# Optimization experiments

Hardware: AMD Instinct MI355X
Metric: run time of the kernel (lower is better)

Reference implementation:

```python
import jax, jax.numpy as jnp
import numpy as np

B, S, D, H = 2, 2048, 1024, 16
HD = D // H


def setup_inputs() -> dict:
    key = jax.random.key(0)
    ks = jax.random.split(key, 6)
    std = 1.0 / np.sqrt(D)
    return {
        "hidden_states": jax.random.normal(ks[0], (B, S, D), dtype=jnp.float32),
        "attention_mask": jnp.zeros((B, 1, S, S), dtype=jnp.float32),
        "Wq": jax.random.normal(ks[1], (D, D), dtype=jnp.float32) * std,
        "bq": jnp.zeros((D,), dtype=jnp.float32),
        "Wk": jax.random.normal(ks[2], (D, D), dtype=jnp.float32) * std,
        "bk": jnp.zeros((D,), dtype=jnp.float32),
        "Wv": jax.random.normal(ks[3], (D, D), dtype=jnp.float32) * std,
        "bv": jnp.zeros((D,), dtype=jnp.float32),
        "Wo": jax.random.normal(ks[4], (D, D), dtype=jnp.float32) * std,
        "bo": jnp.zeros((D,), dtype=jnp.float32),
    }


def reference(hidden_states, attention_mask, Wq, bq, Wk, bk, Wv, bv, Wo, bo):
    scale = HD ** (-0.5)
    # torch Linear: y = x @ W^T + b
    def proj(x, W, b):
        y = jnp.einsum('bsd,ed->bse', x, W) + b
        return y.reshape(B, S, H, HD).transpose(0, 2, 1, 3)  # [B,H,S,HD]
    q = proj(hidden_states, Wq, bq)
    k = proj(hidden_states, Wk, bk)
    v = proj(hidden_states, Wv, bv)
    scores = jnp.einsum('bhqd,bhkd->bhqk', q, k) * scale + attention_mask
    attn = jax.nn.softmax(scores, axis=-1)  # dropout p=0.0 -> identity
    out = jnp.einsum('bhqk,bhkd->bhqd', attn, v)
    out = out.transpose(0, 2, 1, 3).reshape(B, S, D)
    return jnp.einsum('bsd,ed->bse', out, Wo) + bo
```

## Files before the change

### kernel.cpp

```cpp
#include <hip/hip_runtime.h>
#include <hip/hip_bf16.h>
#include <stdint.h>

#define Bb 2
#define Ss 2048
#define Dd 1024
#define Hh 16
#define HD 64

typedef __attribute__((ext_vector_type(8))) __bf16 bf16x8;
typedef __attribute__((ext_vector_type(4))) __bf16 bf16x4;
typedef __attribute__((ext_vector_type(2))) __bf16 bf16x2;
typedef __attribute__((ext_vector_type(4))) float f32x4;
typedef __attribute__((ext_vector_type(16))) float f32x16;

#define LOG2E 1.44269504088896f
#define SCL2 (0.125f * LOG2E)

#define HS_N   (Bb * Ss * Dd)
#define W_N    (Dd * Dd)
#define B_N    (Dd)
#define MS_N   ((long)Bb * Ss * Ss)
#define CAN_HS 0
#define CAN_WQ (CAN_HS + HS_N)
#define CAN_BQ (CAN_WQ + W_N)
#define CAN_WK (CAN_BQ + B_N)
#define CAN_BK (CAN_WK + W_N)
#define CAN_WV (CAN_BK + B_N)
#define CAN_BV (CAN_WV + W_N)
#define CAN_WO (CAN_BV + B_N)
#define CAN_BO (CAN_WO + W_N)
#define CAN_END (CAN_BO + B_N)
#define TSZ    (Bb * Hh * Ss * HD)
#define WS_ELEMS (CAN_END + 4 * TSZ)
#define WS_NEED ((size_t)WS_ELEMS * 2)

__device__ __forceinline__ void gl_lds16(const __bf16* g, __bf16* l) {
  __builtin_amdgcn_global_load_lds(
      (const __attribute__((address_space(1))) void*)g,
      (__attribute__((address_space(3))) void*)l,
      16, 0, 0);
}

__device__ __forceinline__ void cfence() { asm volatile("" ::: "memory"); }

__global__ void canon_kernel(const float* hs, const float* Wq, const float* bq,
                             const float* Wk, const float* bk, const float* Wv,
                             const float* bv, const float* Wo, const float* bo,
                             __bf16* __restrict__ dst) {
  const float* srcs[9] = {hs, Wq, bq, Wk, bk, Wv, bv, Wo, bo};
  const long starts[10] = {CAN_HS, CAN_WQ, CAN_BQ, CAN_WK, CAN_BK,
                           CAN_WV, CAN_BV, CAN_WO, CAN_BO, CAN_END};
  const long nA = CAN_END / 8;
  for (long c = blockIdx.x * blockDim.x + threadIdx.x; c < nA;
       c += (long)gridDim.x * blockDim.x) {
    const long i = c * 8;
    int seg = 0;
#pragma unroll
    for (int t = 1; t < 9; t++) seg += (i >= starts[t]) ? 1 : 0;
    const float* s = srcs[seg] + (i - starts[seg]);
    bf16x8 v;
#pragma unroll
    for (int e = 0; e < 8; e++) v[e] = (__bf16)s[e];
    *(bf16x8*)(dst + i) = v;
  }
}

template <int MODE, typename OutT>
__global__ __launch_bounds__(256, 2) void gemm_bt(
    const __bf16* __restrict__ A,
    const __bf16* __restrict__ W0, const __bf16* __restrict__ W1,
    const __bf16* __restrict__ W2,
    const __bf16* __restrict__ b0, const __bf16* __restrict__ b1,
    const __bf16* __restrict__ b2,
    OutT* __restrict__ O0, OutT* __restrict__ O1, OutT* __restrict__ O2,
    const float* __restrict__ Mf, __bf16* __restrict__ Mout) {
  constexpr int TN = (MODE == 1) ? 64 : 128;
  constexpr int NACC = TN / 32;
  __shared__ __align__(16) __bf16 sA[2][128 * 32];
  __shared__ __align__(16) __bf16 sB[2][TN * 32];
  const int tid = threadIdx.x;

  if (MODE == 0 && blockIdx.y >= 24) {
    const long nT = (long)Bb * 32 * 32 * 256;
    const long t0 = ((long)(blockIdx.y - 24) * 32 + blockIdx.x) * 256 + tid;
    for (long tc = t0; tc < nT; tc += 65536) {
      const int t = (int)(tc & 255);
      const long tile = tc >> 8;
      const int kvt = (int)(tile & 31);
      const int qt = (int)((tile >> 5) & 31);
      const int b = (int)(tile >> 10);
      const int l31 = t & 31, hi5 = (t >> 5) & 1;
      const int qg = (t >> 6) & 1, kvh = (t >> 7) & 1;
      const int q = qt * 64 + qg * 32 + l31;
      const int kv0 = kvt * 64 + kvh * 32 + hi5 * 4;
      const float* src = Mf + ((long)b * Ss + q) * Ss + kv0;
      bf16x8 o0, o1;
#pragma unroll
      for (int g = 0; g < 4; g++) {
        f32x4 v = *(const f32x4*)(src + g * 8);
#pragma unroll
        for (int r = 0; r < 4; r++) {
          const __bf16 w = (__bf16)(v[r] * LOG2E);
          if (g < 2) o0[g * 4 + r] = w;
          else       o1[(g - 2) * 4 + r] = w;
        }
      }
      __bf16* dstp = Mout + (tile << 12) + t * 16;
      *(bf16x8*)(dstp) = o0;
      *(bf16x8*)(dstp + 8) = o1;
    }
    return;
  }

  const int lane = tid & 63;
  const int wid = tid >> 6;
  const int quad = lane >> 4;
  const int l15 = lane & 15;
  const int mBlock = blockIdx.x * 128;

  const __bf16* W;
  const __bf16* bias;
  OutT* Out;
  int nBlock, which = 0;
  if (MODE == 0) {
    which = blockIdx.y >> 3;
    nBlock = (blockIdx.y & 7) * 128;
    W = which == 0 ? W0 : (which == 1 ? W1 : W2);
    bias = which == 0 ? b0 : (which == 1 ? b1 : b2);
    Out = which == 0 ? O0 : (which == 1 ? O1 : O2);
  } else {
    nBlock = blockIdx.y * TN;
    W = W0;
    bias = b0;
    Out = O0;
  }

  const int waveM = (wid >> 1) * 64;
  const int waveN = (wid & 1) * (TN / 2);

  f32x4 acc[4][NACC] = {};

  const int c1 = wid * 64 + lane;
  const int c2 = c1 + 256;
  const __bf16* Ar1 = A + (mBlock + (c1 >> 2)) * Dd + (c1 & 3) * 8;
  const __bf16* Ar2 = A + (mBlock + (c2 >> 2)) * Dd + (c2 & 3) * 8;
  const __bf16* Wr1 = W + (nBlock + (c1 >> 2)) * Dd + (c1 & 3) * 8;
  const __bf16* Wr2 = W + (nBlock + (c2 >> 2)) * Dd + (c2 & 3) * 8;
  const int d1 = (wid * 64) * 8;
  const int d2 = (wid * 64 + 256) * 8;

#define GSTAGE(BI, K0)                                                        \
  {                                                                           \
    gl_lds16(Ar1 + (K0), sA[BI] + d1);                                        \
    gl_lds16(Ar2 + (K0), sA[BI] + d2);                                        \
    gl_lds16(Wr1 + (K0), sB[BI] + d1);                                        \
    if (MODE == 0) gl_lds16(Wr2 + (K0), sB[BI] + d2);                         \
  }

  GSTAGE(0, 0);

#pragma unroll 2
  for (int kt = 0; kt < 32; ++kt) {
    const int bufc = kt & 1;
    __syncthreads();
    if (kt < 31) {
      GSTAGE(bufc ^ 1, (kt + 1) * 32);
    }

    bf16x8 aF[4], bF[NACC];
#pragma unroll
    for (int mi = 0; mi < 4; mi++)
      aF[mi] =
          *(const bf16x8*)(sA[bufc] + (waveM + mi * 16 + l15) * 32 + quad * 8);
#pragma unroll
    for (int ni = 0; ni < NACC; ni++)
      bF[ni] =
          *(const bf16x8*)(sB[bufc] + (waveN + ni * 16 + l15) * 32 + quad * 8);
#pragma unroll
    for (int mi = 0; mi < 4; mi++)
#pragma unroll
      for (int ni = 0; ni < NACC; ni++)
        acc[mi][ni] = __builtin_amdgcn_mfma_f32_16x16x32_bf16(
            aF[mi], bF[ni], acc[mi][ni], 0, 0, 0);
  }

#pragma unroll
  for (int ni = 0; ni < NACC; ni++) {
    const int ng = nBlock + waveN + ni * 16 + l15;
    const float bv = (float)bias[ng];
#pragma unroll
    for (int mi = 0; mi < 4; mi++) {
      const int mg0 = mBlock + waveM + mi * 16 + quad * 4;
      if (MODE == 0 && which == 2) {
        const int b = mg0 >> 11, s0 = mg0 & 2047;
        const int h = ng >> 6, hd = ng & 63;
        bf16x4 pk;
#pragma unroll
        for (int r = 0; r < 4; r++) pk[r] = (__bf16)(acc[mi][ni][r] + bv);
        *(bf16x4*)((__bf16*)Out + (((b * Hh + h) * HD + hd) * Ss) + s0) = pk;
      } else {
#pragma unroll
        for (int r = 0; r < 4; r++) {
          float v = acc[mi][ni][r] + bv;
          const int m = mg0 + r;
          if (MODE == 0) {
            if (which == 0) v *= SCL2;
            const int b = m >> 11, s = m & 2047;
            const int h = ng >> 6, hd = ng & 63;
            Out[(((b * Hh + h) * Ss + s) * HD) + hd] = (OutT)v;
          } else {
            Out[m * Dd + ng] = (OutT)v;
          }
        }
      }
    }
  }
}

__global__ __launch_bounds__(256, 4) void attn_fused(
    const __bf16* __restrict__ Qg, const __bf16* __restrict__ Kg,
    const __bf16* __restrict__ Vt, const __bf16* __restrict__ Mbf,
    __bf16* __restrict__ Og) {
  __shared__ __align__(16) union {
    __bf16 kv[2][8192];
    struct {
      float O[2][64][32];
      float L[2][32];
    } m;
  } sh;

  const int tid = threadIdx.x;
  const int lane = tid & 63;
  const int wid = tid >> 6;
  const int qg = wid & 1;
  const int kvh = wid >> 1;
  const int l31 = lane & 31;
  const int hi = lane >> 5;

  const int id = blockIdx.x;
  const int j = id >> 3;
  const int bh = (id & 7) * 4 + (j >> 5);
  const int qt = j & 31;
  const int qb0 = qt * 64;
  const int b = bh >> 4;
  const int h = bh & 15;
  const int qw = qb0 + qg * 32 + l31;

  const __bf16* Qp = Qg + (size_t)bh * Ss * HD;
  const __bf16* Kp = Kg + (size_t)bh * Ss * HD;
  const __bf16* Vp = Vt + (size_t)bh * HD * Ss;
  const __bf16* Mt = Mbf + (((long)(b * 32 + qt) * 32) << 12) + tid * 16;

  bf16x8 qf[4];
#pragma unroll
  for (int k = 0; k < 4; k++)
    qf[k] = *(const bf16x8*)(Qp + (size_t)qw * HD + k * 16 + hi * 8);

  const int cA = tid, cB = 256 + tid;
#define STAGE_KV(BI, KVS)                                                     \
  {                                                                           \
    const int rwA = (cA & 255) >> 2, rwB = (cB & 255) >> 2;                   \
    const int slA = (cA & 3) ^ ((rwA >> 1) & 3);                              \
    const int slB = (cB & 3) ^ ((rwB >> 1) & 3);                              \
    __bf16* kb = sh.kv[BI];                                                   \
    gl_lds16(Kp + ((KVS) + rwA) * HD + (cA >> 8) * 32 + slA * 8, kb + cA * 8);\
    gl_lds16(Kp + ((KVS) + rwB) * HD + (cB >> 8) * 32 + slB * 8, kb + cB * 8);\
    __bf16* vb = sh.kv[BI] + 4096;                                            \
    gl_lds16(Vp + (size_t)rwA * Ss + (KVS) + (cA >> 8) * 32 + slA * 8,        \
             vb + cA * 8);                                                    \
    gl_lds16(Vp + (size_t)rwB * Ss + (KVS) + (cB >> 8) * 32 + slB * 8,        \
             vb + cB * 8);                                                    \
  }

  f32x16 o[2] = {};
  f32x4 lacc = {0.f, 0.f, 0.f, 0.f};

  const int rsw = (l31 >> 1) & 3;

  bf16x8 mA0, mA1, mB0, mB1;
  mA0 = *(const bf16x8*)(Mt);
  mA1 = *(const bf16x8*)(Mt + 8);
  cfence();
  STAGE_KV(0, 0);
  cfence();
  mB0 = *(const bf16x8*)(Mt + 4096);
  mB1 = *(const bf16x8*)(Mt + 4096 + 8);
  cfence();

#define ATTN_ITER(IT, CUR0, CUR1)                                             \
  {                                                                           \
    const int it = (IT);                                                      \
    const int bufc = it & 1;                                                  \
    cfence();                                                                 \
    if (it == 31)                                                             \
      asm volatile("s_waitcnt vmcnt(0)" ::: "memory");                        \
    else                                                                      \
      asm volatile("s_waitcnt vmcnt(2)" ::: "memory");                        \
    cfence();                                                                 \
    __builtin_amdgcn_s_barrier();                                             \
    cfence();                                                                 \
    f32x16 sacc;                                                              \
    _Pragma("unroll")                                                         \
    for (int e = 0; e < 8; e++) {                                             \
      sacc[e] = (float)CUR0[e];                                               \
      sacc[8 + e] = (float)CUR1[e];                                           \
    }                                                                         \
    cfence();                                                                 \
    if (it < 31) {                                                            \
      STAGE_KV(bufc ^ 1, (it + 1) * 64);                                      \
      cfence();                                                               \
    }                                                                         \
    if (it < 30) {                                                            \
      CUR0 = *(const bf16x8*)(Mt + (it + 2) * 4096);                          \
      CUR1 = *(const bf16x8*)(Mt + (it + 2) * 4096 + 8);                      \
      cfence();                                                               \
    }                                                                         \
    __builtin_amdgcn_s_setprio(1);                                            \
    _Pragma("unroll")                                                         \
    for (int k = 0; k < 4; k++) {                                             \
      const int ps = (((k & 1) << 1) | hi) ^ rsw;                             \
      bf16x8 kf = *(const bf16x8*)(sh.kv[bufc] +                              \
                                   ((k >> 1) * 64 + kvh * 32 + l31) * 32 +    \
                                   ps * 8);                                   \
      sacc =                                                                  \
          __builtin_amdgcn_mfma_f32_32x32x16_bf16(kf, qf[k], sacc, 0, 0, 0);  \
    }                                                                         \
    __builtin_amdgcn_s_setprio(0);                                            \
    f32x4 sv[4];                                                              \
    _Pragma("unroll")                                                         \
    for (int g = 0; g < 4; g++)                                               \
      _Pragma("unroll")                                                       \
      for (int r = 0; r < 4; r++)                                             \
        sv[g][r] = __builtin_amdgcn_exp2f(sacc[g * 4 + r]);                   \
    lacc += (sv[0] + sv[1]) + (sv[2] + sv[3]);                                \
    union pu { bf16x4 v; uint32_t w[2]; };                                    \
    pu pk[4];                                                                 \
    _Pragma("unroll")                                                         \
    for (int g = 0; g < 4; g++)                                               \
      _Pragma("unroll")                                                       \
      for (int r = 0; r < 4; r++) pk[g].v[r] = (__bf16)sv[g][r];              \
    union PF { bf16x8 v; uint32_t u[4]; } pf[2];                              \
    _Pragma("unroll")                                                         \
    for (int ks = 0; ks < 2; ks++) {                                          \
      uint32_t a0 = pk[2 * ks].w[0], b0 = pk[2 * ks + 1].w[0];                \
      uint32_t a1 = pk[2 * ks].w[1], b1 = pk[2 * ks + 1].w[1];                \
      asm volatile("s_nop 1\n\tv_permlane32_swap_b32 %0, %1"                  \
                   : "+v"(a0), "+v"(b0));                                     \
      asm volatile("s_nop 1\n\tv_permlane32_swap_b32 %0, %1"                  \
                   : "+v"(a1), "+v"(b1));                                     \
      pf[ks].u[0] = a0;                                                       \
      pf[ks].u[1] = a1;                                                       \
      pf[ks].u[2] = b0;                                                       \
      pf[ks].u[3] = b1;                                                       \
    }                                                                         \
    __builtin_amdgcn_s_setprio(1);                                            \
    _Pragma("unroll")                                                         \
    for (int k = 0; k < 2; k++)                                               \
      _Pragma("unroll")                                                       \
      for (int hb = 0; hb < 2; hb++) {                                        \
        const int ps = ((k << 1) | hi) ^ rsw;                                 \
        bf16x8 vf = *(const bf16x8*)(sh.kv[bufc] + 4096 +                     \
                                     (kvh * 64 + hb * 32 + l31) * 32 +        \
                                     ps * 8);                                 \
        o[hb] = __builtin_amdgcn_mfma_f32_32x32x16_bf16(vf, pf[k].v, o[hb],   \
                                                        0, 0, 0);             \
      }                                                                       \
    __builtin_amdgcn_s_setprio(0);                                            \
  }

  for (int it2 = 0; it2 < 16; ++it2) {
    ATTN_ITER(2 * it2, mA0, mA1);
    ATTN_ITER(2 * it2 + 1, mB0, mB1);
  }
#undef ATTN_ITER

  float l = lacc[0] + lacc[1] + lacc[2] + lacc[3];
  l += __shfl_xor(l, 32);

  __syncthreads();
  if (kvh == 1) {
#pragma unroll
    for (int hb = 0; hb < 2; hb++)
#pragma unroll
      for (int r = 0; r < 16; r++) {
        const int hd = hb * 32 + (r & 3) + 8 * (r >> 2) + 4 * hi;
        sh.m.O[qg][hd][l31] = o[hb][r];
      }
    if (hi == 0) sh.m.L[qg][l31] = l;
  }
  __syncthreads();
  if (kvh == 0) {
#pragma unroll
    for (int hb = 0; hb < 2; hb++)
#pragma unroll
      for (int r = 0; r < 16; r++) {
        const int hd = hb * 32 + (r & 3) + 8 * (r >> 2) + 4 * hi;
        o[hb][r] += sh.m.O[qg][hd][l31];
      }
    l += sh.m.L[qg][l31];
    const float inv = 1.0f / l;
    __bf16* Ow = Og + (((size_t)b * Ss + qw) * Hh + h) * HD;
#pragma unroll
    for (int hb = 0; hb < 2; hb++)
#pragma unroll
      for (int g = 0; g < 4; g++) {
        const int hd = hb * 32 + g * 8 + 4 * hi;
        bf16x2 w0, w1;
        w0[0] = (__bf16)(o[hb][g * 4 + 0] * inv);
        w0[1] = (__bf16)(o[hb][g * 4 + 1] * inv);
        w1[0] = (__bf16)(o[hb][g * 4 + 2] * inv);
        w1[1] = (__bf16)(o[hb][g * 4 + 3] * inv);
        *(bf16x2*)(Ow + hd) = w0;
        *(bf16x2*)(Ow + hd + 2) = w1;
      }
  }
}

extern "C" void kernel_launch(void* const* d_in, const int* in_sizes, int n_in,
                              void* d_out, int out_size, void* d_ws,
                              size_t ws_size, hipStream_t stream) {
  if (ws_size < WS_NEED) return;

  __bf16* ws = (__bf16*)d_ws;
  const __bf16* hsC = ws + CAN_HS;
  const __bf16* WqC = ws + CAN_WQ;
  const __bf16* bqC = ws + CAN_BQ;
  const __bf16* WkC = ws + CAN_WK;
  const __bf16* bkC = ws + CAN_BK;
  const __bf16* WvC = ws + CAN_WV;
  const __bf16* bvC = ws + CAN_BV;
  const __bf16* WoC = ws + CAN_WO;
  const __bf16* boC = ws + CAN_BO;
  __bf16* Q = ws + CAN_END;
  __bf16* K = Q + TSZ;
  __bf16* V = K + TSZ;
  __bf16* AW = V + TSZ;
  float* out = (float*)d_out;
  __bf16* Mbf = (__bf16*)d_out;

  canon_kernel<<<2048, 256, 0, stream>>>(
      (const float*)d_in[0], (const float*)d_in[2], (const float*)d_in[3],
      (const float*)d_in[4], (const float*)d_in[5], (const float*)d_in[6],
      (const float*)d_in[7], (const float*)d_in[8], (const float*)d_in[9], ws);
  gemm_bt<0, __bf16><<<dim3(32, 32), 256, 0, stream>>>(
      hsC, WqC, WkC, WvC, bqC, bkC, bvC, Q, K, V, (const float*)d_in[1], Mbf);
  attn_fused<<<dim3(1024), 256, 0, stream>>>(Q, K, V, Mbf, AW);
  gemm_bt<1, float><<<dim3(32, 16), 256, 0, stream>>>(
      AW, WoC, WoC, WoC, boC, boC, boC, out, out, out, nullptr, nullptr);
}
```

Measured before the change: 224.8 us.

## Triple-buffer K tiles and prefetch K two iterations ahead in attention

Splits the shared-memory K/V staging into separate buffers: three K buffers and two V buffers. K tiles are now issued two iterations ahead, while V stays one iteration ahead, and the vmcnt wait threshold is raised to match the extra loads in flight. The aim is to hide more global-to-LDS latency for the QK^T MFMA phase. In exchange, LDS per block grows from 32KB to 40KB, which may limit the 4-blocks-per-CU target. The K buffer index is also carried as a runtime variable, adding some address arithmetic.

```diff
diff --git a/kernel.cpp b/kernel.cpp
--- a/kernel.cpp
+++ b/kernel.cpp
@@ -223,7 +223,10 @@
     const __bf16* __restrict__ Vt, const __bf16* __restrict__ Mbf,
     __bf16* __restrict__ Og) {
   __shared__ __align__(16) union {
-    __bf16 kv[2][8192];
+    struct {
+      __bf16 kb[3][4096];
+      __bf16 vb[2][4096];
+    } s;
     struct {
       float O[2][64][32];
       float L[2][32];
@@ -258,19 +261,25 @@
     qf[k] = *(const bf16x8*)(Qp + (size_t)qw * HD + k * 16 + hi * 8);
 
   const int cA = tid, cB = 256 + tid;
-#define STAGE_KV(BI, KVS)                                                     \
+#define STAGE_K(BI, KVS)                                                      \
   {                                                                           \
     const int rwA = (cA & 255) >> 2, rwB = (cB & 255) >> 2;                   \
     const int slA = (cA & 3) ^ ((rwA >> 1) & 3);                              \
     const int slB = (cB & 3) ^ ((rwB >> 1) & 3);                              \
-    __bf16* kb = sh.kv[BI];                                                   \
-    gl_lds16(Kp + ((KVS) + rwA) * HD + (cA >> 8) * 32 + slA * 8, kb + cA * 8);\
-    gl_lds16(Kp + ((KVS) + rwB) * HD + (cB >> 8) * 32 + slB * 8, kb + cB * 8);\
-    __bf16* vb = sh.kv[BI] + 4096;                                            \
+    gl_lds16(Kp + ((KVS) + rwA) * HD + (cA >> 8) * 32 + slA * 8,              \
+             sh.s.kb[BI] + cA * 8);                                           \
+    gl_lds16(Kp + ((KVS) + rwB) * HD + (cB >> 8) * 32 + slB * 8,              \
+             sh.s.kb[BI] + cB * 8);                                           \
+  }
+#define STAGE_V(BI, KVS)                                                      \
+  {                                                                           \
+    const int rwA = (cA & 255) >> 2, rwB = (cB & 255) >> 2;                   \
+    const int slA = (cA & 3) ^ ((rwA >> 1) & 3);                              \
+    const int slB = (cB & 3) ^ ((rwB >> 1) & 3);                              \
     gl_lds16(Vp + (size_t)rwA * Ss + (KVS) + (cA >> 8) * 32 + slA * 8,        \
-             vb + cA * 8);                                                    \
+             sh.s.vb[BI] + cA * 8);                                           \
     gl_lds16(Vp + (size_t)rwB * Ss + (KVS) + (cB >> 8) * 32 + slB * 8,        \
-             vb + cB * 8);                                                    \
+             sh.s.vb[BI] + cB * 8);                                           \
   }
 
   f32x16 o[2] = {};
@@ -279,24 +288,28 @@
   const int rsw = (l31 >> 1) & 3;
 
   bf16x8 mA0, mA1, mB0, mB1;
+  STAGE_K(0, 0);
+  cfence();
   mA0 = *(const bf16x8*)(Mt);
   mA1 = *(const bf16x8*)(Mt + 8);
   cfence();
-  STAGE_KV(0, 0);
+  STAGE_V(0, 0);
+  cfence();
+  STAGE_K(1, 64);
   cfence();
   mB0 = *(const bf16x8*)(Mt + 4096);
   mB1 = *(const bf16x8*)(Mt + 4096 + 8);
   cfence();
 
-#define ATTN_ITER(IT, CUR0, CUR1)                                             \
+#define ATTN_ITER(IT, CUR0, CUR1, KC)                                         \
   {                                                                           \
     const int it = (IT);                                                      \
-    const int bufc = it & 1;                                                  \
+    const int vbc = it & 1;                                                   \
     cfence();                                                                 \
     if (it == 31)                                                             \
       asm volatile("s_waitcnt vmcnt(0)" ::: "memory");                        \
     else                                                                      \
-      asm volatile("s_waitcnt vmcnt(2)" ::: "memory");                        \
+      asm volatile("s_waitcnt vmcnt(4)" ::: "memory");                        \
     cfence();                                                                 \
     __builtin_amdgcn_s_barrier();                                             \
     cfence();                                                                 \
@@ -308,10 +321,13 @@
     }                                                                         \
     cfence();                                                                 \
     if (it < 31) {                                                            \
-      STAGE_KV(bufc ^ 1, (it + 1) * 64);                                      \
+      STAGE_V(vbc ^ 1, (it + 1) * 64);                                        \
       cfence();                                                               \
     }                                                                         \
     if (it < 30) {                                                            \
+      const int kst = (KC) == 0 ? 2 : (KC)-1;                   \
+      STAGE_K(kst, (it + 2) * 64);                                            \
+      cfence();                                                               \
       CUR0 = *(const bf16x8*)(Mt + (it + 2) * 4096);                          \
       CUR1 = *(const bf16x8*)(Mt + (it + 2) * 4096 + 8);                      \
       cfence();                                                               \
@@ -320,7 +336,7 @@
     _Pragma("unroll")                                                         \
     for (int k = 0; k < 4; k++) {                                             \
       const int ps = (((k & 1) << 1) | hi) ^ rsw;                             \
-      bf16x8 kf = *(const bf16x8*)(sh.kv[bufc] +                              \
+      bf16x8 kf = *(const bf16x8*)(sh.s.kb[KC] +                              \
                                    ((k >> 1) * 64 + kvh * 32 + l31) * 32 +    \
                                    ps * 8);                                   \
       sacc =                                                                  \
@@ -360,7 +376,7 @@
       _Pragma("unroll")                                                       \
       for (int hb = 0; hb < 2; hb++) {                                        \
         const int ps = ((k << 1) | hi) ^ rsw;                                 \
-        bf16x8 vf = *(const bf16x8*)(sh.kv[bufc] + 4096 +                     \
+        bf16x8 vf = *(const bf16x8*)(sh.s.vb[vbc] +                           \
                                      (kvh * 64 + hb * 32 + l31) * 32 +        \
                                      ps * 8);                                 \
         o[hb] = __builtin_amdgcn_mfma_f32_32x32x16_bf16(vf, pf[k].v, o[hb],   \
@@ -369,9 +385,12 @@
     __builtin_amdgcn_s_setprio(0);                                            \
   }
 
+  int kc = 0;
   for (int it2 = 0; it2 < 16; ++it2) {
-    ATTN_ITER(2 * it2, mA0, mA1);
-    ATTN_ITER(2 * it2 + 1, mB0, mB1);
+    ATTN_ITER(2 * it2, mA0, mA1, kc);
+    kc = kc == 2 ? 0 : kc + 1;
+    ATTN_ITER(2 * it2 + 1, mB0, mB1, kc);
+    kc = kc == 2 ? 0 : kc + 1;
   }
 #undef ATTN_ITER
 
```

After: 225.2 us. Within noise of the previous version (+0.2%).
